# Optimization experiments

Hardware: AMD Instinct MI355X
Metric: run time of the kernel (lower is better)

## Reference

```python
import jax, jax.numpy as jnp
import numpy as np
from jax.scipy.special import logsumexp

DEPTH = 7
LOG_EPS = jnp.float32(-64.0)
EPS = jnp.float32(np.exp(-64.0))


def leaf_interval(depth, start_idx=0):
    if depth == 0:
        return ([start_idx], [start_idx], [], start_idx)
    l_l, l_r, l_adj, last = leaf_interval(depth - 1, start_idx)
    my = last + 1
    r_l, r_r, r_adj, last = leaf_interval(depth - 1, my + 1)
    return ([my] + l_l, [my] + r_r,
            [(l, r) for l in l_r for r in r_l] + l_adj + r_adj, last)


_start, _end, _adj, _ = leaf_interval(DEPTH)
_out_idx = np.array([i for i, _ in _adj], dtype=np.int32)
OUT_UNIQ, OUT_INV = np.unique(_out_idx, return_inverse=True)
IN_IDX = np.array([j for _, j in _adj], dtype=np.int32)
START_IDXS = np.array(_start, dtype=np.int32)
END_IDXS = np.array(_end, dtype=np.int32)
N_STATES = 2 ** (DEPTH + 1) - 1  # 255


def log_safe(x):
    m = x < EPS
    return jnp.where(m, LOG_EPS, jnp.log(jnp.where(m, EPS, x)))


def exp_safe(x):
    m = x < LOG_EPS
    return jnp.where(m, EPS, jnp.exp(jnp.where(m, LOG_EPS, x)))


def setup_inputs() -> dict:
    key = jax.random.key(0)
    k1, k2, k3 = jax.random.split(key, 3)
    V, B, vocab, T = N_STATES, 64, 5000, 50
    log_probs = jax.nn.log_softmax(
        jax.random.normal(k1, (V, B, vocab), dtype=jnp.float32), axis=-1)
    targets = jax.random.randint(k2, (T, B), 0, vocab)
    target_lengths = jax.random.randint(k3, (B,), 1, T + 1)
    return {"log_probs": log_probs, "targets": targets,
            "target_lengths": target_lengths}


def _forward_ctreec(extracted, target_lengths):
    # extracted: [T, B, V] time-major per-state label log-probs
    T, B, V = extracted.shape
    out_uniq = jnp.asarray(OUT_UNIQ)
    out_inv = jnp.asarray(OUT_INV)
    in_idx = jnp.asarray(IN_IDX)
    end_idxs = jnp.asarray(END_IDXS)
    prev0 = jnp.zeros((B, V), jnp.float32).at[:, jnp.asarray(START_IDXS)].set(1.0)
    acc0 = jnp.zeros((B,), jnp.float32)

    def step(carry, xs):
        prev_probs, acc = carry
        elp_t, t = xs
        log_curr = log_safe(prev_probs) + elp_t            # [B, V]
        log_out = log_curr[:, out_uniq]                    # [B, U] unique out nodes
        log_C = logsumexp(log_out, axis=-1, keepdims=True)  # [B, 1]
        outgoing = exp_safe(log_out - log_C)[:, out_inv]   # [B, E] per-edge probs
        end = (t + 1) == target_lengths                    # [B]
        end_vals = logsumexp(log_curr[:, end_idxs], axis=1)
        acc = acc + jnp.where(end, end_vals, 0.0)
        mid = ((t + 1) < target_lengths) & (t < T - 1)
        acc = acc + jnp.where(mid, log_C[:, 0], 0.0)
        # scatter-add outgoing edge mass onto destination nodes
        new_prev = jnp.zeros_like(prev_probs).at[:, in_idx].add(outgoing)
        return (new_prev, acc), None

    (_, acc), _ = jax.lax.scan(step, (prev0, acc0),
                               (extracted, jnp.arange(T)))
    return acc


def reference(log_probs, targets, target_lengths):
    V, B, vocab = log_probs.shape
    # extracted[t, b, v] = log_probs[v, b, targets[t, b]]
    extracted = log_probs[:, jnp.arange(B)[None, :], targets]  # [V, T, B]
    extracted = jnp.transpose(extracted, (1, 2, 0))            # [T, B, V]
    return -_forward_ctreec(extracted, target_lengths)
```

## Files before the change

### kernel.cpp

```cpp
#include <hip/hip_runtime.h>
#include <math.h>


#define TT 50
#define BB 64
#define VOCAB 5000
#define NS 255
#define NSP 256
#define LOG_EPS_F (-64.0f)
#define EPS_F 1.6038109389511818e-28f
#define WS_NEEDED ((size_t)BB * TT * NSP * 4)

__device__ __forceinline__ float wred_sum(float x) {
#pragma unroll
    for (int m = 32; m >= 1; m >>= 1) x += __shfl_xor(x, m);
    return x;
}
__device__ __forceinline__ float wred_max(float x) {
#pragma unroll
    for (int m = 32; m >= 1; m >>= 1) x = fmaxf(x, __shfl_xor(x, m));
    return x;
}

__global__ __launch_bounds__(256) void gather_kernel(
    const float* __restrict__ log_probs,
    const int* __restrict__ targets,
    const int* __restrict__ target_lengths,
    float* __restrict__ ews)
{
    const int bt = blockIdx.x;
    const int b = bt / TT;
    const int t = bt % TT;
    if (t >= target_lengths[b]) return;
    const int v = threadIdx.x;
    const int tgt = targets[t * BB + b];
    float val = 0.0f;
    if (v < NS)
        val = __expf(log_probs[(size_t)v * (BB * VOCAB) + (size_t)b * VOCAB + tgt]);
    ews[(size_t)bt * NSP + v] = val;
}

__global__ __launch_bounds__(64) void scan_kernel(
    const float* __restrict__ ews,
    const int* __restrict__ target_lengths,
    float* __restrict__ out)
{
    const int b = blockIdx.x;
    const int lane = threadIdx.x;
    const int vbase = lane * 4;
    __shared__ float outv[NSP];

    const int len = target_lengths[b];
    const float4* ew = (const float4*)(ews + (size_t)b * TT * NSP);

    bool isend[4], isout[4];
    int kk[4], jj[4];
    float prev[4];
#pragma unroll
    for (int i = 0; i < 4; ++i) {
        int v = vbase + i;
        int p = v + 1;
        bool valid = (v < NS);
        bool pw2 = (p & (p - 1)) == 0;
        bool e_ = valid && ((p + (p & (-p))) == 256);
        isend[i] = e_;
        isout[i] = valid && !e_;
        prev[i] = (valid && pw2) ? 1.0f : 0.0f;
        if (valid && !pw2) {
            int s = __ffs(p) - 1;
            int q = p & (p - 1);
            kk[i] = __ffs(q) - 1;
            jj[i] = v - (1 << s);
        } else { kk[i] = 0; jj[i] = 0; }
    }

    float acc = 0.0f;
    float4 eA = ew[lane];
    float4 eB = (len > 1) ? ew[64 + lane] : eA;
    for (int t = 0; t < len; ++t) {
        float4 cur = eA;
        eA = eB;
        if (t + 2 < len) eB = ew[(t + 2) * 64 + lane];

        float c[4];
        c[0] = prev[0] * cur.x;
        c[1] = prev[1] * cur.y;
        c[2] = prev[2] * cur.z;
        c[3] = prev[3] * cur.w;

        if (t == len - 1) {
            float s = 0.0f;
#pragma unroll
            for (int i = 0; i < 4; ++i)
                if (isend[i]) s += c[i];
            s = wred_sum(s);
            acc += __logf(s);
        } else {
            *(float4*)&outv[vbase] = make_float4(c[0], c[1], c[2], c[3]);
            float s = 0.0f;
#pragma unroll
            for (int i = 0; i < 4; ++i)
                if (isout[i]) s += c[i];
            s = wred_sum(s);
            acc += __logf(s);
            float rinv = 1.0f / s;
            __syncthreads();
#pragma unroll
            for (int i = 0; i < 4; ++i) {
                float np_ = 0.0f;
                int bj = jj[i];
                int n = kk[i];
                for (int a = 0; a < n; ++a) np_ += outv[bj - (1 << a)];
                prev[i] = np_ * rinv;
            }
            __syncthreads();
        }
    }
    if (lane == 0) out[b] = -acc;
}

__global__ __launch_bounds__(64) void ctreec_fused(
    const float* __restrict__ log_probs,
    const int* __restrict__ targets,
    const int* __restrict__ target_lengths,
    float* __restrict__ out)
{
    const int b = blockIdx.x;
    const int lane = threadIdx.x;
    const int vbase = lane * 4;
    __shared__ float e_lds[TT * NSP];
    __shared__ float outv[NSP];
    __shared__ int tgts[TT];
    const int len = target_lengths[b];
    if (lane < TT) tgts[lane] = targets[lane * BB + b];
    __syncthreads();
    {
        const size_t bvoff = (size_t)b * VOCAB;
        float4* e_vec = (float4*)e_lds;
#pragma unroll 4
        for (int t = 0; t < len; ++t) {
            const float* base = log_probs + bvoff + (size_t)tgts[t];
            float4 val;
            val.x = base[(size_t)(vbase + 0) * (BB * VOCAB)];
            val.y = base[(size_t)(vbase + 1) * (BB * VOCAB)];
            val.z = base[(size_t)(vbase + 2) * (BB * VOCAB)];
            val.w = (vbase + 3 < NS) ? base[(size_t)(vbase + 3) * (BB * VOCAB)] : -1e30f;
            e_vec[t * 64 + lane] = val;
        }
    }
    __syncthreads();
    bool isend[4], isout[4];
    int kk[4], jj[4];
    float prev[4];
#pragma unroll
    for (int i = 0; i < 4; ++i) {
        int v = vbase + i;
        int p = v + 1;
        bool valid = (v < NS);
        bool pw2 = (p & (p - 1)) == 0;
        bool e_ = valid && ((p + (p & (-p))) == 256);
        isend[i] = e_;
        isout[i] = valid && !e_;
        prev[i] = (valid && pw2) ? 1.0f : 0.0f;
        if (valid && !pw2) {
            int s = __ffs(p) - 1;
            int q = p & (p - 1);
            kk[i] = __ffs(q) - 1;
            jj[i] = v - (1 << s);
        } else { kk[i] = 0; jj[i] = 0; }
    }
    const float4* e_vec = (const float4*)e_lds;
    float acc = 0.0f;
    for (int t = 0; t < len; ++t) {
        float4 e4 = e_vec[t * 64 + lane];
        float e[4] = {e4.x, e4.y, e4.z, e4.w};
        float lc[4];
#pragma unroll
        for (int i = 0; i < 4; ++i) {
            float pv = prev[i];
            float lp = (pv < EPS_F) ? LOG_EPS_F : __logf(pv);
            lc[i] = lp + e[i];
        }
        if (t == len - 1) {
            float m = -INFINITY;
#pragma unroll
            for (int i = 0; i < 4; ++i)
                if (isend[i]) m = fmaxf(m, lc[i]);
            m = wred_max(m);
            float s = 0.0f;
#pragma unroll
            for (int i = 0; i < 4; ++i)
                if (isend[i]) s += __expf(lc[i] - m);
            s = wred_sum(s);
            acc += m + __logf(s);
        } else {
            float m = -INFINITY;
#pragma unroll
            for (int i = 0; i < 4; ++i)
                if (isout[i]) m = fmaxf(m, lc[i]);
            m = wred_max(m);
            float s = 0.0f;
#pragma unroll
            for (int i = 0; i < 4; ++i)
                if (isout[i]) s += __expf(lc[i] - m);
            s = wred_sum(s);
            float logC = m + __logf(s);
            acc += logC;
#pragma unroll
            for (int i = 0; i < 4; ++i) {
                float d = lc[i] - logC;
                outv[vbase + i] = (d < LOG_EPS_F) ? EPS_F : __expf(d);
            }
            __syncthreads();
#pragma unroll
            for (int i = 0; i < 4; ++i) {
                float np_ = 0.0f;
                int bj = jj[i];
                int n = kk[i];
                for (int a = 0; a < n; ++a) np_ += outv[bj - (1 << a)];
                prev[i] = np_;
            }
            __syncthreads();
        }
    }
    if (lane == 0) out[b] = -acc;
}

extern "C" void kernel_launch(void* const* d_in, const int* in_sizes, int n_in,
                              void* d_out, int out_size, void* d_ws, size_t ws_size,
                              hipStream_t stream) {
    const float* log_probs = (const float*)d_in[0];
    const int* targets = (const int*)d_in[1];
    const int* target_lengths = (const int*)d_in[2];
    float* out = (float*)d_out;

    if (ws_size >= WS_NEEDED) {
        float* ews = (float*)d_ws;
        gather_kernel<<<dim3(BB * TT), dim3(256), 0, stream>>>(
            log_probs, targets, target_lengths, ews);
        scan_kernel<<<dim3(BB), dim3(64), 0, stream>>>(
            ews, target_lengths, out);
    } else {
        ctreec_fused<<<dim3(BB), dim3(64), 0, stream>>>(
            log_probs, targets, target_lengths, out);
    }
}
```

Before: 441.6 us.

## Fuse gather and scan into one producer-consumer kernel with atomic flags

Replaces the two-kernel gather-then-scan sequence with a single launch. Consumer blocks (one per batch item) spin on a per-batch atomic counter while producer blocks gather and exponentiate rows into workspace and signal completion, so the scan can start as soon as its own batch's rows are ready. This removes a kernel launch boundary and lets gathering overlap with scanning, but adds a memset, spin-waiting that depends on forward-progress ordering of blocks, and fence overhead. The old LDS-based fused fallback is removed, and the two-kernel path becomes the fallback.

After: 510.6 us. 1.16x slower.

```diff
diff --git a/kernel.cpp b/kernel.cpp
--- a/kernel.cpp
+++ b/kernel.cpp
@@ -7,19 +7,126 @@
 #define VOCAB 5000
 #define NS 255
 #define NSP 256
-#define LOG_EPS_F (-64.0f)
-#define EPS_F 1.6038109389511818e-28f
-#define WS_NEEDED ((size_t)BB * TT * NSP * 4)
+
+#define EWS_OFF_BYTES 1024
+#define WS_NEEDED (EWS_OFF_BYTES + (size_t)BB * TT * NSP * 4)
 
 __device__ __forceinline__ float wred_sum(float x) {
 #pragma unroll
     for (int m = 32; m >= 1; m >>= 1) x += __shfl_xor(x, m);
     return x;
 }
-__device__ __forceinline__ float wred_max(float x) {
-#pragma unroll
-    for (int m = 32; m >= 1; m >>= 1) x = fmaxf(x, __shfl_xor(x, m));
-    return x;
+
+__global__ __launch_bounds__(64) void ctreec_fused_pc(
+    const float* __restrict__ log_probs,
+    const int* __restrict__ targets,
+    const int* __restrict__ target_lengths,
+    float* __restrict__ out,
+    unsigned* __restrict__ flags,
+    float* __restrict__ ews)
+{
+    const int bid = blockIdx.x;
+    const int lane = threadIdx.x;
+
+    if (bid >= BB) {
+        const int bt = bid - BB;
+        const int b = bt / TT;
+        const int t = bt % TT;
+        if (t >= target_lengths[b]) return;
+        const int tgt = targets[t * BB + b];
+        const float* base = log_probs + (size_t)b * VOCAB + tgt;
+        float* row = ews + (size_t)bt * NSP;
+#pragma unroll
+        for (int i = 0; i < 4; ++i) {
+            const int v = lane + i * 64;
+            float val = 0.0f;
+            if (v < NS) val = __expf(base[(size_t)v * (BB * VOCAB)]);
+            row[v] = val;
+        }
+        __threadfence();
+        if (lane == 0)
+            __hip_atomic_fetch_add(&flags[b], 1u, __ATOMIC_RELAXED,
+                                   __HIP_MEMORY_SCOPE_AGENT);
+        return;
+    }
+
+    const int b = bid;
+    const int vbase = lane * 4;
+    __shared__ float outv[NSP];
+
+    const int len = target_lengths[b];
+
+    bool isend[4], isout[4];
+    int kk[4], jj[4];
+    float prev[4];
+#pragma unroll
+    for (int i = 0; i < 4; ++i) {
+        int v = vbase + i;
+        int p = v + 1;
+        bool valid = (v < NS);
+        bool pw2 = (p & (p - 1)) == 0;
+        bool e_ = valid && ((p + (p & (-p))) == 256);
+        isend[i] = e_;
+        isout[i] = valid && !e_;
+        prev[i] = (valid && pw2) ? 1.0f : 0.0f;
+        if (valid && !pw2) {
+            int s = __ffs(p) - 1;
+            int q = p & (p - 1);
+            kk[i] = __ffs(q) - 1;
+            jj[i] = v - (1 << s);
+        } else { kk[i] = 0; jj[i] = 0; }
+    }
+
+    while (__hip_atomic_load(&flags[b], __ATOMIC_RELAXED,
+                             __HIP_MEMORY_SCOPE_AGENT) < (unsigned)len)
+        __builtin_amdgcn_s_sleep(8);
+    __threadfence();
+
+    const float4* ew = (const float4*)(ews + (size_t)b * TT * NSP);
+
+    float acc = 0.0f;
+    float4 eA = ew[lane];
+    float4 eB = (len > 1) ? ew[64 + lane] : eA;
+    for (int t = 0; t < len; ++t) {
+        float4 cur = eA;
+        eA = eB;
+        if (t + 2 < len) eB = ew[(t + 2) * 64 + lane];
+
+        float c[4];
+        c[0] = prev[0] * cur.x;
+        c[1] = prev[1] * cur.y;
+        c[2] = prev[2] * cur.z;
+        c[3] = prev[3] * cur.w;
+
+        if (t == len - 1) {
+            float s = 0.0f;
+#pragma unroll
+            for (int i = 0; i < 4; ++i)
+                if (isend[i]) s += c[i];
+            s = wred_sum(s);
+            acc += __logf(s);
+        } else {
+            *(float4*)&outv[vbase] = make_float4(c[0], c[1], c[2], c[3]);
+            float s = 0.0f;
+#pragma unroll
+            for (int i = 0; i < 4; ++i)
+                if (isout[i]) s += c[i];
+            s = wred_sum(s);
+            acc += __logf(s);
+            float rinv = 1.0f / s;
+            __syncthreads();
+#pragma unroll
+            for (int i = 0; i < 4; ++i) {
+                float np_ = 0.0f;
+                int bj = jj[i];
+                int n = kk[i];
+                for (int a = 0; a < n; ++a) np_ += outv[bj - (1 << a)];
+                prev[i] = np_ * rinv;
+            }
+            __syncthreads();
+        }
+    }
+    if (lane == 0) out[b] = -acc;
 }
 
 __global__ __launch_bounds__(256) void gather_kernel(
@@ -49,10 +156,8 @@
     const int lane = threadIdx.x;
     const int vbase = lane * 4;
     __shared__ float outv[NSP];
-
     const int len = target_lengths[b];
     const float4* ew = (const float4*)(ews + (size_t)b * TT * NSP);
-
     bool isend[4], isout[4];
     int kk[4], jj[4];
     float prev[4];
@@ -73,7 +178,6 @@
             jj[i] = v - (1 << s);
         } else { kk[i] = 0; jj[i] = 0; }
     }
-
     float acc = 0.0f;
     float4 eA = ew[lane];
     float4 eB = (len > 1) ? ew[64 + lane] : eA;
@@ -81,13 +185,11 @@
         float4 cur = eA;
         eA = eB;
         if (t + 2 < len) eB = ew[(t + 2) * 64 + lane];
-
         float c[4];
         c[0] = prev[0] * cur.x;
         c[1] = prev[1] * cur.y;
         c[2] = prev[2] * cur.z;
         c[3] = prev[3] * cur.w;
-
         if (t == len - 1) {
             float s = 0.0f;
 #pragma unroll
@@ -119,113 +221,6 @@
     if (lane == 0) out[b] = -acc;
 }
 
-__global__ __launch_bounds__(64) void ctreec_fused(
-    const float* __restrict__ log_probs,
-    const int* __restrict__ targets,
-    const int* __restrict__ target_lengths,
-    float* __restrict__ out)
-{
-    const int b = blockIdx.x;
-    const int lane = threadIdx.x;
-    const int vbase = lane * 4;
-    __shared__ float e_lds[TT * NSP];
-    __shared__ float outv[NSP];
-    __shared__ int tgts[TT];
-    const int len = target_lengths[b];
-    if (lane < TT) tgts[lane] = targets[lane * BB + b];
-    __syncthreads();
-    {
-        const size_t bvoff = (size_t)b * VOCAB;
-        float4* e_vec = (float4*)e_lds;
-#pragma unroll 4
-        for (int t = 0; t < len; ++t) {
-            const float* base = log_probs + bvoff + (size_t)tgts[t];
-            float4 val;
-            val.x = base[(size_t)(vbase + 0) * (BB * VOCAB)];
-            val.y = base[(size_t)(vbase + 1) * (BB * VOCAB)];
-            val.z = base[(size_t)(vbase + 2) * (BB * VOCAB)];
-            val.w = (vbase + 3 < NS) ? base[(size_t)(vbase + 3) * (BB * VOCAB)] : -1e30f;
-            e_vec[t * 64 + lane] = val;
-        }
-    }
-    __syncthreads();
-    bool isend[4], isout[4];
-    int kk[4], jj[4];
-    float prev[4];
-#pragma unroll
-    for (int i = 0; i < 4; ++i) {
-        int v = vbase + i;
-        int p = v + 1;
-        bool valid = (v < NS);
-        bool pw2 = (p & (p - 1)) == 0;
-        bool e_ = valid && ((p + (p & (-p))) == 256);
-        isend[i] = e_;
-        isout[i] = valid && !e_;
-        prev[i] = (valid && pw2) ? 1.0f : 0.0f;
-        if (valid && !pw2) {
-            int s = __ffs(p) - 1;
-            int q = p & (p - 1);
-            kk[i] = __ffs(q) - 1;
-            jj[i] = v - (1 << s);
-        } else { kk[i] = 0; jj[i] = 0; }
-    }
-    const float4* e_vec = (const float4*)e_lds;
-    float acc = 0.0f;
-    for (int t = 0; t < len; ++t) {
-        float4 e4 = e_vec[t * 64 + lane];
-        float e[4] = {e4.x, e4.y, e4.z, e4.w};
-        float lc[4];
-#pragma unroll
-        for (int i = 0; i < 4; ++i) {
-            float pv = prev[i];
-            float lp = (pv < EPS_F) ? LOG_EPS_F : __logf(pv);
-            lc[i] = lp + e[i];
-        }
-        if (t == len - 1) {
-            float m = -INFINITY;
-#pragma unroll
-            for (int i = 0; i < 4; ++i)
-                if (isend[i]) m = fmaxf(m, lc[i]);
-            m = wred_max(m);
-            float s = 0.0f;
-#pragma unroll
-            for (int i = 0; i < 4; ++i)
-                if (isend[i]) s += __expf(lc[i] - m);
-            s = wred_sum(s);
-            acc += m + __logf(s);
-        } else {
-            float m = -INFINITY;
-#pragma unroll
-            for (int i = 0; i < 4; ++i)
-                if (isout[i]) m = fmaxf(m, lc[i]);
-            m = wred_max(m);
-            float s = 0.0f;
-#pragma unroll
-            for (int i = 0; i < 4; ++i)
-                if (isout[i]) s += __expf(lc[i] - m);
-            s = wred_sum(s);
-            float logC = m + __logf(s);
-            acc += logC;
-#pragma unroll
-            for (int i = 0; i < 4; ++i) {
-                float d = lc[i] - logC;
-                outv[vbase + i] = (d < LOG_EPS_F) ? EPS_F : __expf(d);
-            }
-            __syncthreads();
-#pragma unroll
-            for (int i = 0; i < 4; ++i) {
-                float np_ = 0.0f;
-                int bj = jj[i];
-                int n = kk[i];
-                for (int a = 0; a < n; ++a) np_ += outv[bj - (1 << a)];
-                prev[i] = np_;
-            }
-            __syncthreads();
-        }
-    }
-    if (lane == 0) out[b] = -acc;
-}
-
 extern "C" void kernel_launch(void* const* d_in, const int* in_sizes, int n_in,
                               void* d_out, int out_size, void* d_ws, size_t ws_size,
                               hipStream_t stream) {
@@ -235,13 +230,16 @@
     float* out = (float*)d_out;
 
     if (ws_size >= WS_NEEDED) {
+        unsigned* flags = (unsigned*)d_ws;
+        float* ews = (float*)((char*)d_ws + EWS_OFF_BYTES);
+        hipMemsetAsync(d_ws, 0, EWS_OFF_BYTES, stream);
+        ctreec_fused_pc<<<dim3(BB + BB * TT), dim3(64), 0, stream>>>(
+            log_probs, targets, target_lengths, out, flags, ews);
+    } else {
         float* ews = (float*)d_ws;
         gather_kernel<<<dim3(BB * TT), dim3(256), 0, stream>>>(
             log_probs, targets, target_lengths, ews);
         scan_kernel<<<dim3(BB), dim3(64), 0, stream>>>(
             ews, target_lengths, out);
-    } else {
-        ctreec_fused<<<dim3(BB), dim3(64), 0, stream>>>(
-            log_probs, targets, target_lengths, out);
-    }
-}
+    }
+}
```
